# Kernel tuning notes

Hardware: AMD Instinct MI355X
Metric: run time of the kernel (lower is better)

Reference implementation:

```python
import jax, jax.numpy as jnp
import numpy as np

N_HEAD = 16
N_EMBD = 1024
BLOCK = 2048
B, T = 4, 2048


def setup_inputs() -> dict:
    key = jax.random.key(0)
    ks = jax.random.split(key, 5)
    scale = 1.0 / np.sqrt(N_EMBD)
    return {
        "x": jax.random.normal(ks[0], (B, T, N_EMBD), dtype=jnp.float32),
        "W_attn": jax.random.normal(ks[1], (N_EMBD, 3 * N_EMBD), dtype=jnp.float32) * scale,
        "b_attn": jax.random.normal(ks[2], (3 * N_EMBD,), dtype=jnp.float32) * 0.02,
        "W_proj": jax.random.normal(ks[3], (N_EMBD, N_EMBD), dtype=jnp.float32) * scale,
        "b_proj": jax.random.normal(ks[4], (N_EMBD,), dtype=jnp.float32) * 0.02,
    }


def reference(x, W_attn, b_attn, W_proj, b_proj):
    Bb, Tt, C = x.shape
    hd = C // N_HEAD
    qkv = x @ W_attn + b_attn                      # [B,T,3C]
    q, k, v = jnp.split(qkv, 3, axis=2)
    # [B,H,T,hd]
    q = q.reshape(Bb, Tt, N_HEAD, hd).transpose(0, 2, 1, 3)
    k = k.reshape(Bb, Tt, N_HEAD, hd).transpose(0, 2, 1, 3)
    v = v.reshape(Bb, Tt, N_HEAD, hd).transpose(0, 2, 1, 3)
    att = jnp.einsum('bhqd,bhkd->bhqk', q, k) / np.sqrt(hd).astype(x.dtype)
    causal = jnp.tril(jnp.ones((Tt, Tt), dtype=bool))
    att = jnp.where(causal[None, None], att, jnp.finfo(att.dtype).min)
    att = jax.nn.softmax(att, axis=-1)
    y = jnp.einsum('bhqk,bhkd->bhqd', att, v)      # [B,H,T,hd]
    y = y.transpose(0, 2, 1, 3).reshape(Bb, Tt, C)
    return y @ W_proj + b_proj
```

## Files before the change

kernel.cpp:

```cpp
#include <hip/hip_runtime.h>
#include <stdint.h>

typedef unsigned short u16;
typedef __bf16 bf16;
typedef bf16 bf16x8 __attribute__((ext_vector_type(8)));
typedef float f32x4 __attribute__((ext_vector_type(4)));
typedef u16 u16x8 __attribute__((ext_vector_type(8)));
typedef u16 u16x4 __attribute__((ext_vector_type(4)));

#define T_SEQ 2048
#define NHEAD 16
#define HD    64
#define CEMB  1024
#define QS    8388608
#define QSCALE 0.18033688011112042f

#define BARRIER() asm volatile("s_barrier" ::: "memory")
#define WAITV(N)  asm volatile("s_waitcnt vmcnt(" #N ")" ::: "memory")

__device__ __forceinline__ u16 f2b(float f){
  bf16 h = (bf16)f;
  return __builtin_bit_cast(u16, h);
}
__device__ __forceinline__ void glds16(const void* g, const void* l){
  __builtin_amdgcn_global_load_lds(
    (__attribute__((address_space(1))) unsigned int*)(uintptr_t)g,
    (__attribute__((address_space(3))) unsigned int*)(uintptr_t)l,
    16, 0, 0);
}

__global__ __launch_bounds__(256) void prep_kernel(
    const float* __restrict__ x, u16* __restrict__ xb,
    const float* __restrict__ Wa, u16* __restrict__ Wta,
    const float* __restrict__ Wp, u16* __restrict__ Wtp)
{
  __shared__ __align__(16) u16 tile[64][72];
  const int bid = blockIdx.x;
  const int tid = threadIdx.x;
  if (bid < 4096){
    const int i = (bid * 256 + tid) * 8;
    f32x4 a = *(const f32x4*)&x[i];
    f32x4 b = *(const f32x4*)&x[i + 4];
    u16x8 h;
    #pragma unroll
    for (int j = 0; j < 4; j++){ h[j] = f2b(a[j]); h[4+j] = f2b(b[j]); }
    *(u16x8*)&xb[i] = h;
    return;
  }
  const float* src; u16* dst; int K, N, bx, by;
  if (bid < 4864){ const int j = bid - 4096; src = Wa; dst = Wta; K = 1024; N = 3072; bx = j % 48; by = j / 48; }
  else           { const int j = bid - 4864; src = Wp; dst = Wtp; K = 1024; N = 1024; bx = j % 16; by = j / 16; }
  const int n0 = bx * 64, k0 = by * 64;
  #pragma unroll
  for (int it = 0; it < 4; it++){
    const int idx = it * 256 + tid;
    const int row = idx >> 4, c4 = (idx & 15) * 4;
    f32x4 v = *(const f32x4*)&src[(size_t)(k0 + row) * N + n0 + c4];
    #pragma unroll
    for (int j = 0; j < 4; j++) tile[row][c4 + j] = f2b(v[j]);
  }
  __syncthreads();
  const int r = tid >> 3, cc = (tid & 7) * 8;
  #pragma unroll
  for (int i = 0; i < 2; i++){
    const int rr = r + i * 32;
    u16x8 v;
    #pragma unroll
    for (int j = 0; j < 8; j++) v[j] = tile[cc + j][rr];
    *(u16x8*)&dst[(size_t)(n0 + rr) * K + k0 + cc] = v;
  }
}

#define QSTAGE(BUF, K0) do{ \
  _Pragma("unroll") \
  for (int ii = 0; ii < 4; ii++){ \
    const int slot0 = (wave*4 + ii) * 64; \
    const int s = slot0 + lane; \
    const int row = s >> 3; \
    const int cc8 = ((s & 7) ^ (row & 7)) * 8; \
    glds16(&A [(size_t)(m0 + row) * Ktot + (K0) + cc8], &As[BUF][slot0*8]); \
    glds16(&Bt[(size_t)(n0 + row) * Ktot + (K0) + cc8], &Bs[BUF][slot0*8]); \
  } \
}while(0)

__global__ __launch_bounds__(256) void gemm_qkv128(
    const u16* __restrict__ A, const u16* __restrict__ Bt,
    const float* __restrict__ bias, u16* __restrict__ out, int Ktot)
{
  __shared__ __align__(16) u16 As[2][128*64];
  __shared__ __align__(16) u16 Bs[2][128*64];
  const int tid = threadIdx.x;
  const int lane = tid & 63, wave = tid >> 6;
  const int l15 = lane & 15, l4 = lane >> 4;
  const int wm = wave >> 1, wn = wave & 1;
  const int id = blockIdx.x;
  const int swz = (id & 7) * 192 + (id >> 3);
  const int m0 = (swz / 24) * 128, n0 = (swz % 24) * 128;
  const int NT = Ktot >> 6;

  f32x4 acc[4][4] = {};

  QSTAGE(0, 0);
  for (int c = 0; c < NT; c++){
    const int cur = c & 1;
    if (c + 1 < NT){
      QSTAGE(cur ^ 1, (c + 1) * 64);
      WAITV(8);
    } else {
      WAITV(0);
    }
    BARRIER();

    #pragma unroll
    for (int ks = 0; ks < 2; ks++){
      bf16x8 af[4], bfr[4];
      #pragma unroll
      for (int mt = 0; mt < 4; mt++){
        const int rf = wm*64 + mt*16 + l15;
        const int slot = rf*8 + ((ks*4 + l4) ^ (rf & 7));
        af[mt] = *(const bf16x8*)&As[cur][slot*8];
      }
      #pragma unroll
      for (int nt = 0; nt < 4; nt++){
        const int rf = wn*64 + nt*16 + l15;
        const int slot = rf*8 + ((ks*4 + l4) ^ (rf & 7));
        bfr[nt] = *(const bf16x8*)&Bs[cur][slot*8];
      }
      #pragma unroll
      for (int mt = 0; mt < 4; mt++)
        #pragma unroll
        for (int nt = 0; nt < 4; nt++)
          acc[mt][nt] = __builtin_amdgcn_mfma_f32_16x16x32_bf16(
              af[mt], bfr[nt], acc[mt][nt], 0, 0, 0);
    }
    BARRIER();
  }

  #pragma unroll
  for (int nt = 0; nt < 4; nt++){
    const int n = n0 + wn*64 + nt*16 + l15;
    const float bias_v = bias[n];
    const int which = n >> 10;
    const int cc = n & 1023;
    const int h = cc >> 6, d = cc & 63;
    const float sc = (which == 0) ? QSCALE : 1.0f;
    if (which == 2){
      #pragma unroll
      for (int mt = 0; mt < 4; mt++){
        const int rowg = m0 + wm*64 + mt*16 + l4*4;
        const int bb = rowg >> 11, t = rowg & 2047;
        u16x4 pk;
        #pragma unroll
        for (int r = 0; r < 4; r++) pk[r] = f2b(acc[mt][nt][r] + bias_v);
        *(u16x4*)&out[(size_t)2*QS + ((size_t)(bb*NHEAD + h)*HD + d)*T_SEQ + t] = pk;
      }
    } else {
      #pragma unroll
      for (int mt = 0; mt < 4; mt++)
        #pragma unroll
        for (int r = 0; r < 4; r++){
          const int rowg = m0 + wm*64 + mt*16 + l4*4 + r;
          const int bb = rowg >> 11, t = rowg & 2047;
          out[(size_t)which*QS + ((size_t)(bb*NHEAD + h)*T_SEQ + t)*HD + d]
              = f2b((acc[mt][nt][r] + bias_v) * sc);
        }
    }
  }
}

__global__ __launch_bounds__(256) void gemm_proj(
    const u16* __restrict__ A, const u16* __restrict__ Bt,
    const float* __restrict__ bias, float* __restrict__ out, int Ktot)
{
  __shared__ __align__(16) u16 As[2][128*64];
  __shared__ __align__(16) u16 Bs[2][128*64];
  const int tid = threadIdx.x;
  const int lane = tid & 63, wave = tid >> 6;
  const int l15 = lane & 15, l4 = lane >> 4;
  const int wm = wave >> 1, wn = wave & 1;
  const int id = blockIdx.x;
  const int swz = (id & 7) * 64 + (id >> 3);
  const int m0 = (swz / 8) * 128, n0 = (swz % 8) * 128;
  const int NT = Ktot >> 6;

  f32x4 acc[4][4] = {};

  QSTAGE(0, 0);
  for (int c = 0; c < NT; c++){
    const int cur = c & 1;
    if (c + 1 < NT){
      QSTAGE(cur ^ 1, (c + 1) * 64);
      WAITV(8);
    } else {
      WAITV(0);
    }
    BARRIER();

    #pragma unroll
    for (int ks = 0; ks < 2; ks++){
      bf16x8 af[4], bfr[4];
      #pragma unroll
      for (int mt = 0; mt < 4; mt++){
        const int rf = wm*64 + mt*16 + l15;
        const int slot = rf*8 + ((ks*4 + l4) ^ (rf & 7));
        af[mt] = *(const bf16x8*)&As[cur][slot*8];
      }
      #pragma unroll
      for (int nt = 0; nt < 4; nt++){
        const int rf = wn*64 + nt*16 + l15;
        const int slot = rf*8 + ((ks*4 + l4) ^ (rf & 7));
        bfr[nt] = *(const bf16x8*)&Bs[cur][slot*8];
      }
      #pragma unroll
      for (int mt = 0; mt < 4; mt++)
        #pragma unroll
        for (int nt = 0; nt < 4; nt++)
          acc[mt][nt] = __builtin_amdgcn_mfma_f32_16x16x32_bf16(
              af[mt], bfr[nt], acc[mt][nt], 0, 0, 0);
    }
    BARRIER();
  }

  #pragma unroll
  for (int nt = 0; nt < 4; nt++){
    const int n = n0 + wn*64 + nt*16 + l15;
    const float bias_v = bias[n];
    #pragma unroll
    for (int mt = 0; mt < 4; mt++)
      #pragma unroll
      for (int r = 0; r < 4; r++){
        const int rowg = m0 + wm*64 + mt*16 + l4*4 + r;
        out[(size_t)rowg*CEMB + n] = acc[mt][nt][r] + bias_v;
      }
  }
}

__global__ __launch_bounds__(256, 3) void attn_kernel(
    const u16* __restrict__ qb, const u16* __restrict__ kb,
    const u16* __restrict__ vtb, u16* __restrict__ y)
{
  __shared__ __align__(16) u16 Ks[2*64*64];
  __shared__ __align__(16) u16 Vt[2*64*64];
  __shared__ __align__(16) u16 Pw[8*16*72];
  const int tid = threadIdx.x;
  const int lane = tid & 63, wave = tid >> 6;
  const int l15 = lane & 15, l4 = lane >> 4;
  const int qt = 15 - (blockIdx.x >> 6);
  const int bh = blockIdx.x & 63;
  const int q0 = qt * 128;
  const size_t base = (size_t)bh * (T_SEQ * HD);
  const u16* qp  = qb  + base;
  const u16* kp  = kb  + base;
  const u16* vtp = vtb + base;

  const int qmin0 = q0 + wave*32;
  const int qmin1 = qmin0 + 16;

  bf16x8 qf[2][2];
  #pragma unroll
  for (int g = 0; g < 2; g++){
    const int m = qmin0 + g*16 + l15;
    qf[g][0] = *(const bf16x8*)&qp[m*HD +      l4*8];
    qf[g][1] = *(const bf16x8*)&qp[m*HD + 32 + l4*8];
  }
  f32x4 o[2][4] = {};
  float l_run[2] = {0.f, 0.f};

  const int s0i = (wave*2 + 0) * 64 + lane;
  const int s1i = (wave*2 + 1) * 64 + lane;
  const int row0 = s0i >> 3, c0 = (s0i & 7) ^ (row0 & 7);
  const int row1 = s1i >> 3, c1 = (s1i & 7) ^ (row1 & 7);
  const int koff0 = row0*HD + c0*8, koff1 = row1*HD + c1*8;
  const int voff0 = row0*T_SEQ + c0*8, voff1 = row1*T_SEQ + c1*8;
  const int ldso0 = (wave*2 + 0) * 64 * 8, ldso1 = (wave*2 + 1) * 64 * 8;

  const int nkt = 2*qt + 2;

  glds16(&kp [koff0], &Ks[ldso0]);
  glds16(&kp [koff1], &Ks[ldso1]);
  glds16(&vtp[voff0], &Vt[ldso0]);
  glds16(&vtp[voff1], &Vt[ldso1]);

  for (int kt = 0; kt < nkt; kt++){
    const int cb = (kt & 1) * 4096;
    if (kt + 1 < nkt){
      const int nb = ((kt + 1) & 1) * 4096;
      glds16(&kp [(kt+1)*4096 + koff0], &Ks[nb + ldso0]);
      glds16(&kp [(kt+1)*4096 + koff1], &Ks[nb + ldso1]);
      glds16(&vtp[(kt+1)*64   + voff0], &Vt[nb + ldso0]);
      glds16(&vtp[(kt+1)*64   + voff1], &Vt[nb + ldso1]);
      WAITV(4);
    } else {
      WAITV(0);
    }
    BARRIER();

    const int t0 = kt*64;
    if (t0 <= qmin1 + 15){
      const bool act0 = (t0 <= qmin0 + 15);

      f32x4 s0[4], s1[4];
      #pragma unroll
      for (int nb2 = 0; nb2 < 4; nb2++){
        f32x4 a0 = {}, a1 = {};
        #pragma unroll
        for (int ks = 0; ks < 2; ks++){
          const int rf = nb2*16 + l15;
          const int slot = rf*8 + ((ks*4 + l4) ^ (rf & 7));
          bf16x8 kf = *(const bf16x8*)&Ks[cb + slot*8];
          a1 = __builtin_amdgcn_mfma_f32_16x16x32_bf16(kf, qf[1][ks], a1, 0, 0, 0);
          if (act0)
            a0 = __builtin_amdgcn_mfma_f32_16x16x32_bf16(kf, qf[0][ks], a0, 0, 0, 0);
        }
        s1[nb2] = a1; s0[nb2] = a0;
      }

      #pragma unroll
      for (int g = 0; g < 2; g++){
        if (g == 0 && !act0) continue;
        f32x4* sf = (g == 0) ? s0 : s1;
        const int qmin = (g == 0) ? qmin0 : qmin1;
        const int qg = qmin + l15;
        float lsum = 0.f;
        if (t0 + 63 > qmin){
          #pragma unroll
          for (int nb2 = 0; nb2 < 4; nb2++){
            u16x4 pk;
            #pragma unroll
            for (int r = 0; r < 4; r++){
              const int t = t0 + nb2*16 + l4*4 + r;
              float p = __builtin_amdgcn_exp2f(sf[nb2][r]);
              p = (t <= qg) ? p : 0.0f;
              lsum += p;
              pk[r] = f2b(p);
            }
            *(u16x4*)&Pw[(wave*2 + g)*1152 + l15*72 + nb2*16 + l4*4] = pk;
          }
        } else {
          #pragma unroll
          for (int nb2 = 0; nb2 < 4; nb2++){
            u16x4 pk;
            #pragma unroll
            for (int r = 0; r < 4; r++){
              const float p = __builtin_amdgcn_exp2f(sf[nb2][r]);
              lsum += p;
              pk[r] = f2b(p);
            }
            *(u16x4*)&Pw[(wave*2 + g)*1152 + l15*72 + nb2*16 + l4*4] = pk;
          }
        }
        l_run[g] += lsum;
      }

      #pragma unroll
      for (int ks = 0; ks < 2; ks++){
        bf16x8 pf1 = *(const bf16x8*)&Pw[(wave*2 + 1)*1152 + l15*72 + ks*32 + l4*8];
        bf16x8 pf0;
        if (act0) pf0 = *(const bf16x8*)&Pw[(wave*2 + 0)*1152 + l15*72 + ks*32 + l4*8];
        #pragma unroll
        for (int nh = 0; nh < 4; nh++){
          const int rf = nh*16 + l15;
          const int slot = rf*8 + ((ks*4 + l4) ^ (rf & 7));
          bf16x8 vf = *(const bf16x8*)&Vt[cb + slot*8];
          o[1][nh] = __builtin_amdgcn_mfma_f32_16x16x32_bf16(vf, pf1, o[1][nh], 0, 0, 0);
          if (act0)
            o[0][nh] = __builtin_amdgcn_mfma_f32_16x16x32_bf16(vf, pf0, o[0][nh], 0, 0, 0);
        }
      }
    }
    BARRIER();
  }

  const int b = bh >> 4, h = bh & 15;
  #pragma unroll
  for (int g = 0; g < 2; g++){
    float lr = l_run[g];
    lr += __shfl_xor(lr, 16);
    lr += __shfl_xor(lr, 32);
    const float inv_l = 1.0f / lr;
    const int t = qmin0 + g*16 + l15;
    #pragma unroll
    for (int nh = 0; nh < 4; nh++){
      u16x4 pk;
      #pragma unroll
      for (int r = 0; r < 4; r++) pk[r] = f2b(o[g][nh][r] * inv_l);
      *(u16x4*)&y[((size_t)(b*T_SEQ + t))*CEMB + h*HD + nh*16 + l4*4] = pk;
    }
  }
}

extern "C" void kernel_launch(void* const* d_in, const int* in_sizes, int n_in,
                              void* d_out, int out_size, void* d_ws, size_t ws_size,
                              hipStream_t stream) {
  const float* x      = (const float*)d_in[0];
  const float* W_attn = (const float*)d_in[1];
  const float* b_attn = (const float*)d_in[2];
  const float* W_proj = (const float*)d_in[3];
  const float* b_proj = (const float*)d_in[4];
  float* out = (float*)d_out;
  u16* ws  = (u16*)d_ws;

  u16* Wt_attn = ws;
  u16* Wt_proj = ws + 3145728;
  u16* xb      = ws + 4194304;
  u16* qkv     = ws + 12582912;
  u16* y       = xb;

  prep_kernel<<<5120, 256, 0, stream>>>(x, xb, W_attn, Wt_attn, W_proj, Wt_proj);
  gemm_qkv128<<<1536, 256, 0, stream>>>(xb, Wt_attn, b_attn, qkv, 1024);
  attn_kernel<<<1024, 256, 0, stream>>>(qkv, qkv + QS, qkv + 2*QS, y);
  gemm_proj<<<512, 256, 0, stream>>>(y, Wt_proj, b_proj, out, 1024);
}
```

Baseline: 226.9 us.

## Load K/V fragments directly from global in attention, drop LDS staging and GEMM swizzle

The attention kernel no longer double-buffers K and V^T tiles in shared memory with async global-to-LDS copies and barriers. Each wave now reads its MFMA fragments straight from global memory and loops only over its own causal range, with no block-wide synchronisation. This removes barrier stalls and LDS traffic, but gives up K/V reuse across the four waves and the latency hiding of the prefetch. The QKV GEMM's block-index swizzle is also replaced with a plain row-major tile mapping, which may reduce L2 locality.

Measured after the change: 318.9 us. +40.6%, slower.

```diff
diff --git a/kernel.cpp b/kernel.cpp
--- a/kernel.cpp
+++ b/kernel.cpp
@@ -94,8 +94,7 @@
   const int l15 = lane & 15, l4 = lane >> 4;
   const int wm = wave >> 1, wn = wave & 1;
   const int id = blockIdx.x;
-  const int swz = (id & 7) * 192 + (id >> 3);
-  const int m0 = (swz / 24) * 128, n0 = (swz % 24) * 128;
+  const int m0 = (id / 24) * 128, n0 = (id % 24) * 128;
   const int NT = Ktot >> 6;
 
   f32x4 acc[4][4] = {};
@@ -239,8 +238,6 @@
     const u16* __restrict__ qb, const u16* __restrict__ kb,
     const u16* __restrict__ vtb, u16* __restrict__ y)
 {
-  __shared__ __align__(16) u16 Ks[2*64*64];
-  __shared__ __align__(16) u16 Vt[2*64*64];
   __shared__ __align__(16) u16 Pw[8*16*72];
   const int tid = threadIdx.x;
   const int lane = tid & 63, wave = tid >> 6;
@@ -266,109 +263,78 @@
   f32x4 o[2][4] = {};
   float l_run[2] = {0.f, 0.f};
 
-  const int s0i = (wave*2 + 0) * 64 + lane;
-  const int s1i = (wave*2 + 1) * 64 + lane;
-  const int row0 = s0i >> 3, c0 = (s0i & 7) ^ (row0 & 7);
-  const int row1 = s1i >> 3, c1 = (s1i & 7) ^ (row1 & 7);
-  const int koff0 = row0*HD + c0*8, koff1 = row1*HD + c1*8;
-  const int voff0 = row0*T_SEQ + c0*8, voff1 = row1*T_SEQ + c1*8;
-  const int ldso0 = (wave*2 + 0) * 64 * 8, ldso1 = (wave*2 + 1) * 64 * 8;
-
-  const int nkt = 2*qt + 2;
-
-  glds16(&kp [koff0], &Ks[ldso0]);
-  glds16(&kp [koff1], &Ks[ldso1]);
-  glds16(&vtp[voff0], &Vt[ldso0]);
-  glds16(&vtp[voff1], &Vt[ldso1]);
-
-  for (int kt = 0; kt < nkt; kt++){
-    const int cb = (kt & 1) * 4096;
-    if (kt + 1 < nkt){
-      const int nb = ((kt + 1) & 1) * 4096;
-      glds16(&kp [(kt+1)*4096 + koff0], &Ks[nb + ldso0]);
-      glds16(&kp [(kt+1)*4096 + koff1], &Ks[nb + ldso1]);
-      glds16(&vtp[(kt+1)*64   + voff0], &Vt[nb + ldso0]);
-      glds16(&vtp[(kt+1)*64   + voff1], &Vt[nb + ldso1]);
-      WAITV(4);
-    } else {
-      WAITV(0);
-    }
-    BARRIER();
-
+  const int kmax = (qmin1 + 15) >> 6;
+  const int krow = l15*HD    + l4*8;
+  const int vrow = l15*T_SEQ + l4*8;
+
+  for (int kt = 0; kt <= kmax; kt++){
     const int t0 = kt*64;
-    if (t0 <= qmin1 + 15){
-      const bool act0 = (t0 <= qmin0 + 15);
-
-      f32x4 s0[4], s1[4];
-      #pragma unroll
-      for (int nb2 = 0; nb2 < 4; nb2++){
-        f32x4 a0 = {}, a1 = {};
-        #pragma unroll
-        for (int ks = 0; ks < 2; ks++){
-          const int rf = nb2*16 + l15;
-          const int slot = rf*8 + ((ks*4 + l4) ^ (rf & 7));
-          bf16x8 kf = *(const bf16x8*)&Ks[cb + slot*8];
-          a1 = __builtin_amdgcn_mfma_f32_16x16x32_bf16(kf, qf[1][ks], a1, 0, 0, 0);
-          if (act0)
-            a0 = __builtin_amdgcn_mfma_f32_16x16x32_bf16(kf, qf[0][ks], a0, 0, 0, 0);
+    const bool act0 = (t0 <= qmin0 + 15);
+
+    f32x4 s0[4], s1[4];
+    #pragma unroll
+    for (int nb2 = 0; nb2 < 4; nb2++){
+      f32x4 a0 = {}, a1 = {};
+      #pragma unroll
+      for (int ks = 0; ks < 2; ks++){
+        bf16x8 kf = *(const bf16x8*)&kp[(t0 + nb2*16)*HD + krow + ks*32];
+        a1 = __builtin_amdgcn_mfma_f32_16x16x32_bf16(kf, qf[1][ks], a1, 0, 0, 0);
+        if (act0)
+          a0 = __builtin_amdgcn_mfma_f32_16x16x32_bf16(kf, qf[0][ks], a0, 0, 0, 0);
+      }
+      s1[nb2] = a1; s0[nb2] = a0;
+    }
+
+    #pragma unroll
+    for (int g = 0; g < 2; g++){
+      if (g == 0 && !act0) continue;
+      f32x4* sf = (g == 0) ? s0 : s1;
+      const int qmin = (g == 0) ? qmin0 : qmin1;
+      const int qg = qmin + l15;
+      float lsum = 0.f;
+      if (t0 + 63 > qmin){
+        #pragma unroll
+        for (int nb2 = 0; nb2 < 4; nb2++){
+          u16x4 pk;
+          #pragma unroll
+          for (int r = 0; r < 4; r++){
+            const int t = t0 + nb2*16 + l4*4 + r;
+            float p = __builtin_amdgcn_exp2f(sf[nb2][r]);
+            p = (t <= qg) ? p : 0.0f;
+            lsum += p;
+            pk[r] = f2b(p);
+          }
+          *(u16x4*)&Pw[(wave*2 + g)*1152 + l15*72 + nb2*16 + l4*4] = pk;
         }
-        s1[nb2] = a1; s0[nb2] = a0;
-      }
-
-      #pragma unroll
-      for (int g = 0; g < 2; g++){
-        if (g == 0 && !act0) continue;
-        f32x4* sf = (g == 0) ? s0 : s1;
-        const int qmin = (g == 0) ? qmin0 : qmin1;
-        const int qg = qmin + l15;
-        float lsum = 0.f;
-        if (t0 + 63 > qmin){
+      } else {
+        #pragma unroll
+        for (int nb2 = 0; nb2 < 4; nb2++){
+          u16x4 pk;
           #pragma unroll
-          for (int nb2 = 0; nb2 < 4; nb2++){
-            u16x4 pk;
-            #pragma unroll
-            for (int r = 0; r < 4; r++){
-              const int t = t0 + nb2*16 + l4*4 + r;
-              float p = __builtin_amdgcn_exp2f(sf[nb2][r]);
-              p = (t <= qg) ? p : 0.0f;
-              lsum += p;
-              pk[r] = f2b(p);
-            }
-            *(u16x4*)&Pw[(wave*2 + g)*1152 + l15*72 + nb2*16 + l4*4] = pk;
+          for (int r = 0; r < 4; r++){
+            const float p = __builtin_amdgcn_exp2f(sf[nb2][r]);
+            lsum += p;
+            pk[r] = f2b(p);
           }
-        } else {
-          #pragma unroll
-          for (int nb2 = 0; nb2 < 4; nb2++){
-            u16x4 pk;
-            #pragma unroll
-            for (int r = 0; r < 4; r++){
-              const float p = __builtin_amdgcn_exp2f(sf[nb2][r]);
-              lsum += p;
-              pk[r] = f2b(p);
-            }
-            *(u16x4*)&Pw[(wave*2 + g)*1152 + l15*72 + nb2*16 + l4*4] = pk;
-          }
+          *(u16x4*)&Pw[(wave*2 + g)*1152 + l15*72 + nb2*16 + l4*4] = pk;
         }
-        l_run[g] += lsum;
-      }
-
-      #pragma unroll
-      for (int ks = 0; ks < 2; ks++){
-        bf16x8 pf1 = *(const bf16x8*)&Pw[(wave*2 + 1)*1152 + l15*72 + ks*32 + l4*8];
-        bf16x8 pf0;
-        if (act0) pf0 = *(const bf16x8*)&Pw[(wave*2 + 0)*1152 + l15*72 + ks*32 + l4*8];
-        #pragma unroll
-        for (int nh = 0; nh < 4; nh++){
-          const int rf = nh*16 + l15;
-          const int slot = rf*8 + ((ks*4 + l4) ^ (rf & 7));
-          bf16x8 vf = *(const bf16x8*)&Vt[cb + slot*8];
-          o[1][nh] = __builtin_amdgcn_mfma_f32_16x16x32_bf16(vf, pf1, o[1][nh], 0, 0, 0);
-          if (act0)
-            o[0][nh] = __builtin_amdgcn_mfma_f32_16x16x32_bf16(vf, pf0, o[0][nh], 0, 0, 0);
-        }
-      }
-    }
-    BARRIER();
+      }
+      l_run[g] += lsum;
+    }
+
+    #pragma unroll
+    for (int ks = 0; ks < 2; ks++){
+      bf16x8 pf1 = *(const bf16x8*)&Pw[(wave*2 + 1)*1152 + l15*72 + ks*32 + l4*8];
+      bf16x8 pf0;
+      if (act0) pf0 = *(const bf16x8*)&Pw[(wave*2 + 0)*1152 + l15*72 + ks*32 + l4*8];
+      #pragma unroll
+      for (int nh = 0; nh < 4; nh++){
+        bf16x8 vf = *(const bf16x8*)&vtp[(size_t)(nh*16)*T_SEQ + vrow + t0 + ks*32];
+        o[1][nh] = __builtin_amdgcn_mfma_f32_16x16x32_bf16(vf, pf1, o[1][nh], 0, 0, 0);
+        if (act0)
+          o[0][nh] = __builtin_amdgcn_mfma_f32_16x16x32_bf16(vf, pf0, o[0][nh], 0, 0, 0);
+      }
+    }
   }
 
   const int b = bh >> 4, h = bh & 15;
```
